# Kernel tuning notes

Measured on AMD Instinct MI355X. Metric: run time of the kernel, lower is better.

## Reference

```python
import jax, jax.numpy as jnp
import numpy as np

N_NODES = 100000
N_EDGES = 1600000
D = 128
NEG_SLOPE = 0.01  # torch F.leaky_relu default


def setup_inputs() -> dict:
    key = jax.random.key(0)
    k1, k2, k3, k4, k5, k6 = jax.random.split(key, 6)
    input = jax.random.normal(k1, (N_NODES, D), dtype=jnp.float32)
    edge_row = jax.random.randint(k2, (N_EDGES,), 0, N_NODES, dtype=jnp.int32)
    edge_col = jax.random.randint(k3, (N_EDGES,), 0, N_NODES, dtype=jnp.int32)
    edge_val = jax.random.uniform(k4, (N_EDGES,), dtype=jnp.float32)
    # learned params: W1: Linear(D, D, bias=False), W2: Linear(2D, D, bias=False)
    # torch stores weight as [out, in]; apply as x @ W.T
    bound1 = 1.0 / np.sqrt(D)
    bound2 = 1.0 / np.sqrt(2 * D)
    W1 = jax.random.uniform(k5, (D, D), dtype=jnp.float32, minval=-bound1, maxval=bound1)
    W2 = jax.random.uniform(k6, (D, 2 * D), dtype=jnp.float32, minval=-bound2, maxval=bound2)
    return {"input": input, "edge_row": edge_row, "edge_col": edge_col,
            "edge_val": edge_val, "W1": W1, "W2": W2}


def reference(input, edge_row, edge_col, edge_val, W1, W2):
    # proj_input = W1(input)
    proj = input @ W1.T                                   # [N, D]
    # neighboor = spmm(adj, proj): out[i] = sum_e val[e] * proj[col[e]] for row[e]==i
    msg = edge_val[:, None] * proj[edge_col]              # [E, D]
    neigh = jax.ops.segment_sum(msg, edge_row, num_segments=input.shape[0])  # [N, D]
    h = jnp.concatenate([input + neigh, input * neigh], axis=-1)  # [N, 2D]
    return jax.nn.leaky_relu(h @ W2.T, NEG_SLOPE)         # [N, D]
```

## Files before the change

### kernel.cpp

```cpp
#include <hip/hip_runtime.h>

#define DIM 128
#define BROWS 128
#define BCAP 3072
#define BK_EDGES 2048

typedef __attribute__((ext_vector_type(8))) short short8;
typedef __attribute__((ext_vector_type(4))) float f32x4;

__device__ __forceinline__ unsigned short f2bf(float f) {
    unsigned u = __float_as_uint(f);
    u += 0x7fffu + ((u >> 16) & 1u);
    return (unsigned short)(u >> 16);
}
__device__ __forceinline__ float bf2f(unsigned short b) {
    return __uint_as_float(((unsigned)b) << 16);
}

__global__ void k_pre(const float4* __restrict__ in, const float* __restrict__ W1,
                      const float* __restrict__ W2, unsigned short* __restrict__ inputb,
                      unsigned short* __restrict__ w1b, unsigned short* __restrict__ w2b,
                      int* __restrict__ gcur, int n4, int nCvt, int nbuk) {
    int b = blockIdx.x;
    if (b < nCvt) {
        int i = b * 256 + threadIdx.x;
        if (i < n4) {
            float4 v = in[i];
            *(ushort4*)(inputb + (long)i * 4) =
                make_ushort4(f2bf(v.x), f2bf(v.y), f2bf(v.z), f2bf(v.w));
        }
    } else if (b < nCvt + 192) {
        int idx = (b - nCvt) * 256 + threadIdx.x;
        if (idx < 16384)      w1b[idx] = f2bf(W1[idx]);
        else                  w2b[idx - 16384] = f2bf(W2[idx - 16384]);
    } else {
        int i = (b - nCvt - 192) * 256 + threadIdx.x;
        if (i < nbuk) gcur[i] = 0;
    }
}

__global__ __launch_bounds__(256) void k_bucket(const int* __restrict__ er,
                                                const int* __restrict__ ec,
                                                const float* __restrict__ ev,
                                                int* __restrict__ gcur,
                                                int2* __restrict__ edata, int E, int nbuk) {
    __shared__ int lhist[800];
    __shared__ int lpos[800];
    for (int b = threadIdx.x; b < nbuk; b += 256) lhist[b] = 0;
    __syncthreads();
    int e0 = blockIdx.x * BK_EDGES;
    for (int j = 0; j < BK_EDGES; j += 256) {
        int e = e0 + j + threadIdx.x;
        if (e < E) atomicAdd(&lhist[er[e] >> 7], 1);
    }
    __syncthreads();
    for (int b = threadIdx.x; b < nbuk; b += 256) {
        int c = lhist[b];
        int g = (c > 0) ? atomicAdd(&gcur[b], c) : 0;
        lpos[b] = b * BCAP + g;
    }
    __syncthreads();
    for (int j = 0; j < BK_EDGES; j += 256) {
        int e = e0 + j + threadIdx.x;
        if (e < E) {
            int r = er[e], b = r >> 7;
            int p = atomicAdd(&lpos[b], 1);
            if (p < (b + 1) * BCAP)
                edata[p] = make_int2(((r & 127) << 17) | ec[e], __float_as_int(ev[e]));
        }
    }
}

__global__ __launch_bounds__(256) void k_csr(int2* __restrict__ edata,
                                             const int* __restrict__ gcur,
                                             int* __restrict__ rs, int* __restrict__ re) {
    __shared__ int2 sed[BCAP];
    __shared__ int hist[BROWS];
    __shared__ int scan[BROWS];
    __shared__ int lcur[BROWS];
    int b = blockIdx.x, tid = threadIdx.x;
    int cnt = gcur[b]; if (cnt > BCAP) cnt = BCAP;
    int2* ed = edata + (long)b * BCAP;
    if (tid < BROWS) hist[tid] = 0;
    for (int i = tid; i < cnt; i += 256) sed[i] = ed[i];
    __syncthreads();
    for (int i = tid; i < cnt; i += 256) atomicAdd(&hist[sed[i].x >> 17], 1);
    __syncthreads();
    if (tid < BROWS) scan[tid] = hist[tid];
    __syncthreads();
    for (int off = 1; off < BROWS; off <<= 1) {
        int v = (tid < BROWS && tid >= off) ? scan[tid - off] : 0;
        __syncthreads();
        if (tid < BROWS) scan[tid] += v;
        __syncthreads();
    }
    if (tid < BROWS) {
        int excl = scan[tid] - hist[tid];
        lcur[tid] = excl;
        int row = b * BROWS + tid;
        rs[row] = b * BCAP + excl;
        re[row] = b * BCAP + excl + hist[tid];
    }
    __syncthreads();
    for (int i = tid; i < cnt; i += 256) {
        int2 v = sed[i];
        int p = atomicAdd(&lcur[v.x >> 17], 1);
        ed[p] = make_int2(v.x & 0x1FFFF, v.y);
    }
}

__global__ __launch_bounds__(256) void k_gather(const unsigned short* __restrict__ xb,
                                                const int2* __restrict__ edata,
                                                const int* __restrict__ rs,
                                                const int* __restrict__ re,
                                                unsigned short* __restrict__ aggb, int N) {
    int tid = threadIdx.x, lane = tid & 63, wave = tid >> 6;
    int grp = lane >> 4, s = lane & 15;
    int row = blockIdx.x * 16 + wave * 4 + grp;
    int beg = 0, end = 0;
    if (row < N) { beg = rs[row]; end = re[row]; }
    int deg = end - beg;
    int m = deg;
    m = max(m, __shfl_xor(m, 16));
    m = max(m, __shfl_xor(m, 32));
    float pa[8];
#pragma unroll
    for (int k = 0; k < 8; ++k) pa[k] = 0.f;
    const int4* x4 = (const int4*)xb;
    int bsrc = lane & 48;

#define ACC8(U, V)                                                         \
    {                                                                      \
        const unsigned* wp_ = (const unsigned*)&(U);                       \
        pa[0] += (V) * __uint_as_float(wp_[0] << 16);                      \
        pa[1] += (V) * __uint_as_float(wp_[0] & 0xffff0000u);              \
        pa[2] += (V) * __uint_as_float(wp_[1] << 16);                      \
        pa[3] += (V) * __uint_as_float(wp_[1] & 0xffff0000u);              \
        pa[4] += (V) * __uint_as_float(wp_[2] << 16);                      \
        pa[5] += (V) * __uint_as_float(wp_[2] & 0xffff0000u);              \
        pa[6] += (V) * __uint_as_float(wp_[3] << 16);                      \
        pa[7] += (V) * __uint_as_float(wp_[3] & 0xffff0000u);              \
    }

    for (int c0 = 0; c0 < m; c0 += 16) {
        int idx = beg + c0 + s;
        int2 ed = (idx < end) ? edata[idx] : make_int2(0, 0);
        int nc = m - c0; if (nc > 16) nc = 16;
        nc = (nc + 3) & ~3;
        for (int j = 0; j < nc; j += 4) {
            int cx0 = __shfl(ed.x, bsrc + j);
            int cx1 = __shfl(ed.x, bsrc + j + 1);
            int cx2 = __shfl(ed.x, bsrc + j + 2);
            int cx3 = __shfl(ed.x, bsrc + j + 3);
            float v0 = __int_as_float(__shfl(ed.y, bsrc + j));
            float v1 = __int_as_float(__shfl(ed.y, bsrc + j + 1));
            float v2 = __int_as_float(__shfl(ed.y, bsrc + j + 2));
            float v3 = __int_as_float(__shfl(ed.y, bsrc + j + 3));
            int4 u0 = x4[(long)cx0 * 16 + s];
            int4 u1 = x4[(long)cx1 * 16 + s];
            int4 u2 = x4[(long)cx2 * 16 + s];
            int4 u3 = x4[(long)cx3 * 16 + s];
            ACC8(u0, v0);
            ACC8(u1, v1);
            ACC8(u2, v2);
            ACC8(u3, v3);
        }
    }
#undef ACC8

    if (row < N) {
        short8 o;
#pragma unroll
        for (int k = 0; k < 8; ++k) o[k] = (short)f2bf(pa[k]);
        *(short8*)(aggb + (long)row * DIM + s * 8) = o;
    }
}

__global__ __launch_bounds__(256, 4) void k_fused(const unsigned short* __restrict__ aggb,
                                                  const unsigned short* __restrict__ inputb,
                                                  const unsigned short* __restrict__ w1b,
                                                  const unsigned short* __restrict__ w2b,
                                                  float* __restrict__ out, int N) {
    __shared__ __align__(16) unsigned short sh[2 * 64 * 136];
    int w = threadIdx.x >> 6, lane = threadIdx.x & 63;
    int quad = lane >> 4, lq = lane & 15;
    int blk0 = blockIdx.x * 64;
    unsigned short* sh0 = sh;
    unsigned short* sh1 = sh + 64 * 136;

    short8 b1[2][4];
#pragma unroll
    for (int ntl = 0; ntl < 2; ++ntl)
#pragma unroll
        for (int kb = 0; kb < 4; ++kb)
            b1[ntl][kb] = *(const short8*)(w1b + ((w * 2 + ntl) * 16 + lq) * DIM +
                                           kb * 32 + quad * 8);

#pragma unroll
    for (int mt = 0; mt < 4; ++mt) {
        short8 afr[4];
        {
            int row = blk0 + mt * 16 + lq; if (row >= N) row = N - 1;
#pragma unroll
            for (int kb = 0; kb < 4; ++kb)
                afr[kb] = *(const short8*)(aggb + (long)row * DIM + kb * 32 + quad * 8);
        }
#pragma unroll
        for (int ntl = 0; ntl < 2; ++ntl) {
            f32x4 c = {0.f, 0.f, 0.f, 0.f};
#pragma unroll
            for (int kb = 0; kb < 4; ++kb)
                c = __builtin_amdgcn_mfma_f32_16x16x32_bf16(afr[kb], b1[ntl][kb], c, 0, 0, 0);
            int nt = w * 2 + ntl;
#pragma unroll
            for (int rg = 0; rg < 4; ++rg) {
                int r = blk0 + mt * 16 + quad * 4 + rg;
                int rr = (r < N) ? r : (N - 1);
                float x = bf2f(inputb[(long)rr * DIM + nt * 16 + lq]);
                float nb = c[rg];
                int off = (mt * 16 + quad * 4 + rg) * 136 + nt * 16 + lq;
                sh0[off] = f2bf(x + nb);
                sh1[off] = f2bf(x * nb);
            }
        }
    }

    short8 b2[2][8];
#pragma unroll
    for (int ntl = 0; ntl < 2; ++ntl)
#pragma unroll
        for (int kb = 0; kb < 8; ++kb)
            b2[ntl][kb] = *(const short8*)(w2b + ((w * 2 + ntl) * 16 + lq) * 256 +
                                           kb * 32 + quad * 8);
    __syncthreads();

#pragma unroll
    for (int mt = 0; mt < 4; ++mt) {
        int arow = (mt * 16 + lq) * 136;
        short8 a0[4], a1[4];
#pragma unroll
        for (int kb = 0; kb < 4; ++kb) {
            a0[kb] = *(const short8*)(sh0 + arow + kb * 32 + quad * 8);
            a1[kb] = *(const short8*)(sh1 + arow + kb * 32 + quad * 8);
        }
#pragma unroll
        for (int ntl = 0; ntl < 2; ++ntl) {
            f32x4 c = {0.f, 0.f, 0.f, 0.f};
#pragma unroll
            for (int kb = 0; kb < 4; ++kb)
                c = __builtin_amdgcn_mfma_f32_16x16x32_bf16(a0[kb], b2[ntl][kb], c, 0, 0, 0);
#pragma unroll
            for (int kb = 0; kb < 4; ++kb)
                c = __builtin_amdgcn_mfma_f32_16x16x32_bf16(a1[kb], b2[ntl][kb + 4], c, 0, 0, 0);
            int nt = w * 2 + ntl;
#pragma unroll
            for (int rg = 0; rg < 4; ++rg) {
                int r = blk0 + mt * 16 + quad * 4 + rg;
                if (r < N) {
                    float v = c[rg];
                    v = (v > 0.f) ? v : 0.01f * v;
                    out[(long)r * DIM + nt * 16 + lq] = v;
                }
            }
        }
    }
}

extern "C" void kernel_launch(void* const* d_in, const int* in_sizes, int n_in,
                              void* d_out, int out_size, void* d_ws, size_t ws_size,
                              hipStream_t stream) {
    const float* input = (const float*)d_in[0];
    const int*   er    = (const int*)d_in[1];
    const int*   ec    = (const int*)d_in[2];
    const float* ev    = (const float*)d_in[3];
    const float* W1    = (const float*)d_in[4];
    const float* W2    = (const float*)d_in[5];
    int N = in_sizes[0] / DIM;
    int E = in_sizes[1];
    float* out = (float*)d_out;
    int nbuk = (N + BROWS - 1) / BROWS;

    int* ws = (int*)d_ws;
    int* gcur = ws;
    int2* edata = (int2*)(ws + 1024);
    int* rs = (int*)(edata + (long)nbuk * BCAP);
    int* re = rs + (long)nbuk * BROWS;
    unsigned short* w1b = (unsigned short*)(re + (long)nbuk * BROWS);
    unsigned short* w2b = w1b + 16384;
    unsigned short* inputb = w2b + 32768;
    unsigned short* aggb = inputb + (long)N * DIM;

    int n4 = N * (DIM / 4);
    int nCvt = (n4 + 255) / 256;
    int nZero = (nbuk + 255) / 256;
    k_pre<<<nCvt + 192 + nZero, 256, 0, stream>>>(
        (const float4*)input, W1, W2, inputb, w1b, w2b, gcur, n4, nCvt, nbuk);

    k_bucket<<<(E + BK_EDGES - 1) / BK_EDGES, 256, 0, stream>>>(
        er, ec, ev, gcur, edata, E, nbuk);

    k_csr<<<nbuk, 256, 0, stream>>>(edata, gcur, rs, re);

    k_gather<<<(N + 15) / 16, 256, 0, stream>>>(inputb, edata, rs, re, aggb, N);

    k_fused<<<(N + 63) / 64, 256, 0, stream>>>(aggb, inputb, w1b, w2b, out, N);
}
```

Baseline: 275.9 us.

## Use coarse 1024-row buckets and compact CSR output into dense edge array

Edges are now bucketed by groups of 1024 rows (98 buckets) into a temporary staging area that aliases the aggregation buffer. The CSR kernel then runs with 1024 threads per bucket and computes each bucket's global base with a serial prefix over the bucket counts. It scatters edges into a compact, densely packed edge array instead of padded per-bucket slots. This cuts global atomic contention and shrinks the bucket-histogram work, and it gives the gather kernel contiguous edges. The costs are far fewer CSR blocks (98, so low occupancy), per-thread global re-reads instead of shared-memory staging, and reliance on a fixed bucket capacity that may overflow on skewed inputs.

```diff
diff --git a/kernel.cpp b/kernel.cpp
--- a/kernel.cpp
+++ b/kernel.cpp
@@ -1,8 +1,8 @@
 #include <hip/hip_runtime.h>
 
 #define DIM 128
-#define BROWS 128
-#define BCAP 3072
+#define CB_ROWS 1024
+#define CCAP 18432
 #define BK_EDGES 2048
 
 typedef __attribute__((ext_vector_type(8))) short short8;
@@ -43,69 +43,76 @@
                                                 const int* __restrict__ ec,
                                                 const float* __restrict__ ev,
                                                 int* __restrict__ gcur,
-                                                int2* __restrict__ edata, int E, int nbuk) {
-    __shared__ int lhist[800];
-    __shared__ int lpos[800];
-    for (int b = threadIdx.x; b < nbuk; b += 256) lhist[b] = 0;
+                                                int2* __restrict__ edata0, int E, int nbuk) {
+    __shared__ int lhist[128];
+    __shared__ int lpos[128];
+    if (threadIdx.x < 128) lhist[threadIdx.x] = 0;
     __syncthreads();
     int e0 = blockIdx.x * BK_EDGES;
     for (int j = 0; j < BK_EDGES; j += 256) {
         int e = e0 + j + threadIdx.x;
-        if (e < E) atomicAdd(&lhist[er[e] >> 7], 1);
-    }
-    __syncthreads();
-    for (int b = threadIdx.x; b < nbuk; b += 256) {
-        int c = lhist[b];
-        int g = (c > 0) ? atomicAdd(&gcur[b], c) : 0;
-        lpos[b] = b * BCAP + g;
+        if (e < E) atomicAdd(&lhist[er[e] >> 10], 1);
+    }
+    __syncthreads();
+    if (threadIdx.x < nbuk) {
+        int c = lhist[threadIdx.x];
+        int g = (c > 0) ? atomicAdd(&gcur[threadIdx.x], c) : 0;
+        lpos[threadIdx.x] = threadIdx.x * CCAP + g;
     }
     __syncthreads();
     for (int j = 0; j < BK_EDGES; j += 256) {
         int e = e0 + j + threadIdx.x;
         if (e < E) {
-            int r = er[e], b = r >> 7;
+            int r = er[e], b = r >> 10;
             int p = atomicAdd(&lpos[b], 1);
-            if (p < (b + 1) * BCAP)
-                edata[p] = make_int2(((r & 127) << 17) | ec[e], __float_as_int(ev[e]));
-        }
-    }
-}
-
-__global__ __launch_bounds__(256) void k_csr(int2* __restrict__ edata,
-                                             const int* __restrict__ gcur,
-                                             int* __restrict__ rs, int* __restrict__ re) {
-    __shared__ int2 sed[BCAP];
-    __shared__ int hist[BROWS];
-    __shared__ int scan[BROWS];
-    __shared__ int lcur[BROWS];
+            if (p < (b + 1) * CCAP)
+                edata0[p] = make_int2(((r & 1023) << 17) | ec[e], __float_as_int(ev[e]));
+        }
+    }
+}
+
+__global__ __launch_bounds__(1024) void k_csr(const int2* __restrict__ edata0,
+                                              const int* __restrict__ gcur,
+                                              int2* __restrict__ edata,
+                                              int* __restrict__ rs, int* __restrict__ re,
+                                              int N, int nbuk) {
+    __shared__ int hist[CB_ROWS];
+    __shared__ int scan[CB_ROWS];
+    __shared__ int lcur[CB_ROWS];
+    __shared__ int cbuf[128];
+    __shared__ int cbase;
     int b = blockIdx.x, tid = threadIdx.x;
-    int cnt = gcur[b]; if (cnt > BCAP) cnt = BCAP;
-    int2* ed = edata + (long)b * BCAP;
-    if (tid < BROWS) hist[tid] = 0;
-    for (int i = tid; i < cnt; i += 256) sed[i] = ed[i];
-    __syncthreads();
-    for (int i = tid; i < cnt; i += 256) atomicAdd(&hist[sed[i].x >> 17], 1);
-    __syncthreads();
-    if (tid < BROWS) scan[tid] = hist[tid];
-    __syncthreads();
-    for (int off = 1; off < BROWS; off <<= 1) {
-        int v = (tid < BROWS && tid >= off) ? scan[tid - off] : 0;
+    if (tid < nbuk) { int c = gcur[tid]; cbuf[tid] = (c > CCAP) ? CCAP : c; }
+    hist[tid] = 0;
+    __syncthreads();
+    if (tid == 0) {
+        int s = 0;
+        for (int i = 0; i < b; ++i) s += cbuf[i];
+        cbase = s;
+    }
+    __syncthreads();
+    int base = cbase;
+    int cnt = cbuf[b];
+    const int2* e0 = edata0 + (long)b * CCAP;
+    for (int i = tid; i < cnt; i += 1024) atomicAdd(&hist[e0[i].x >> 17], 1);
+    __syncthreads();
+    scan[tid] = hist[tid];
+    __syncthreads();
+    for (int off = 1; off < CB_ROWS; off <<= 1) {
+        int v = (tid >= off) ? scan[tid - off] : 0;
         __syncthreads();
-        if (tid < BROWS) scan[tid] += v;
+        scan[tid] += v;
         __syncthreads();
     }
-    if (tid < BROWS) {
-        int excl = scan[tid] - hist[tid];
-        lcur[tid] = excl;
-        int row = b * BROWS + tid;
-        rs[row] = b * BCAP + excl;
-        re[row] = b * BCAP + excl + hist[tid];
-    }
-    __syncthreads();
-    for (int i = tid; i < cnt; i += 256) {
-        int2 v = sed[i];
+    int excl = scan[tid] - hist[tid];
+    lcur[tid] = base + excl;
+    int row = b * CB_ROWS + tid;
+    if (row < N) { rs[row] = base + excl; re[row] = base + excl + hist[tid]; }
+    __syncthreads();
+    for (int i = tid; i < cnt; i += 1024) {
+        int2 v = e0[i];
         int p = atomicAdd(&lcur[v.x >> 17], 1);
-        ed[p] = make_int2(v.x & 0x1FFFF, v.y);
+        edata[p] = make_int2(v.x & 0x1FFFF, v.y);
     }
 }
 
@@ -278,17 +285,18 @@
     int N = in_sizes[0] / DIM;
     int E = in_sizes[1];
     float* out = (float*)d_out;
-    int nbuk = (N + BROWS - 1) / BROWS;
+    int nbuk = (N + CB_ROWS - 1) / CB_ROWS;
 
     int* ws = (int*)d_ws;
     int* gcur = ws;
     int2* edata = (int2*)(ws + 1024);
-    int* rs = (int*)(edata + (long)nbuk * BCAP);
-    int* re = rs + (long)nbuk * BROWS;
-    unsigned short* w1b = (unsigned short*)(re + (long)nbuk * BROWS);
+    int* rs = (int*)(edata + (long)E);
+    int* re = rs + N;
+    unsigned short* w1b = (unsigned short*)(re + N);
     unsigned short* w2b = w1b + 16384;
     unsigned short* inputb = w2b + 32768;
     unsigned short* aggb = inputb + (long)N * DIM;
+    int2* edata0 = (int2*)aggb;
 
     int n4 = N * (DIM / 4);
     int nCvt = (n4 + 255) / 256;
@@ -297,9 +305,9 @@
         (const float4*)input, W1, W2, inputb, w1b, w2b, gcur, n4, nCvt, nbuk);
 
     k_bucket<<<(E + BK_EDGES - 1) / BK_EDGES, 256, 0, stream>>>(
-        er, ec, ev, gcur, edata, E, nbuk);
-
-    k_csr<<<nbuk, 256, 0, stream>>>(edata, gcur, rs, re);
+        er, ec, ev, gcur, edata0, E, nbuk);
+
+    k_csr<<<nbuk, 1024, 0, stream>>>(edata0, gcur, edata, rs, re, N, nbuk);
 
     k_gather<<<(N + 15) / 16, 256, 0, stream>>>(inputb, edata, rs, re, aggb, N);
 
```

Measured after the change: 276.9 us. Within noise of the previous version (+0.4%).

## Fuse CSR build into gather and stage bucket writes through shared memory

Applied to the files above, without the earlier changes.

The bucketing kernel now uses 1024-thread blocks over 6144 edges. It locally sorts edges by bucket in LDS via a prefix scan, then writes each bucket's run contiguously to global memory for coalesced stores. The separate CSR kernel is removed. Its per-row sort now runs inside the gather kernel, which keeps the sorted edge list in LDS and processes all 128 rows of a bucket per block. This drops one launch and the global round-trip of rs/re and reordered edata, at the cost of only nbuk (~782) gather blocks with serialized per-row loops, which may reduce parallelism and load balance.

```diff
diff --git a/kernel.cpp b/kernel.cpp
--- a/kernel.cpp
+++ b/kernel.cpp
@@ -3,7 +3,8 @@
 #define DIM 128
 #define BROWS 128
 #define BCAP 3072
-#define BK_EDGES 2048
+#define NBUK_PAD 800
+#define BK_EDGES 6144
 
 typedef __attribute__((ext_vector_type(8))) short short8;
 typedef __attribute__((ext_vector_type(4))) float f32x4;
@@ -39,95 +40,92 @@
     }
 }
 
-__global__ __launch_bounds__(256) void k_bucket(const int* __restrict__ er,
-                                                const int* __restrict__ ec,
-                                                const float* __restrict__ ev,
-                                                int* __restrict__ gcur,
-                                                int2* __restrict__ edata, int E, int nbuk) {
-    __shared__ int lhist[800];
-    __shared__ int lpos[800];
-    for (int b = threadIdx.x; b < nbuk; b += 256) lhist[b] = 0;
+__global__ __launch_bounds__(1024) void k_bucket(const int* __restrict__ er,
+                                                 const int* __restrict__ ec,
+                                                 const float* __restrict__ ev,
+                                                 int* __restrict__ gcur,
+                                                 int2* __restrict__ edata0, int E, int nbuk) {
+    __shared__ int2 sed[BK_EDGES];
+    __shared__ int lhist[NBUK_PAD];
+    __shared__ int lscan[NBUK_PAD];
+    __shared__ int lpos[NBUK_PAD];
+    __shared__ int gbase[NBUK_PAD];
+    int tid = threadIdx.x;
+    if (tid < NBUK_PAD) lhist[tid] = 0;
     __syncthreads();
     int e0 = blockIdx.x * BK_EDGES;
-    for (int j = 0; j < BK_EDGES; j += 256) {
-        int e = e0 + j + threadIdx.x;
-        if (e < E) atomicAdd(&lhist[er[e] >> 7], 1);
-    }
-    __syncthreads();
-    for (int b = threadIdx.x; b < nbuk; b += 256) {
-        int c = lhist[b];
-        int g = (c > 0) ? atomicAdd(&gcur[b], c) : 0;
-        lpos[b] = b * BCAP + g;
-    }
-    __syncthreads();
-    for (int j = 0; j < BK_EDGES; j += 256) {
-        int e = e0 + j + threadIdx.x;
-        if (e < E) {
-            int r = er[e], b = r >> 7;
-            int p = atomicAdd(&lpos[b], 1);
-            if (p < (b + 1) * BCAP)
-                edata[p] = make_int2(((r & 127) << 17) | ec[e], __float_as_int(ev[e]));
-        }
-    }
-}
-
-__global__ __launch_bounds__(256) void k_csr(int2* __restrict__ edata,
-                                             const int* __restrict__ gcur,
-                                             int* __restrict__ rs, int* __restrict__ re) {
+    int bcnt = E - e0; if (bcnt > BK_EDGES) bcnt = BK_EDGES;
+    for (int i = tid; i < bcnt; i += 1024)
+        atomicAdd(&lhist[er[e0 + i] >> 7], 1);
+    __syncthreads();
+    if (tid < NBUK_PAD) lscan[tid] = lhist[tid];
+    __syncthreads();
+    for (int off = 1; off < NBUK_PAD; off <<= 1) {
+        int v = (tid < NBUK_PAD && tid >= off) ? lscan[tid - off] : 0;
+        __syncthreads();
+        if (tid < NBUK_PAD) lscan[tid] += v;
+        __syncthreads();
+    }
+    if (tid < NBUK_PAD) {
+        int c = lhist[tid];
+        lpos[tid] = lscan[tid] - c;
+        gbase[tid] = (c > 0 && tid < nbuk) ? atomicAdd(&gcur[tid], c) : 0;
+    }
+    __syncthreads();
+    for (int i = tid; i < bcnt; i += 1024) {
+        int e = e0 + i;
+        int r = er[e], bk = r >> 7;
+        int p = atomicAdd(&lpos[bk], 1);
+        sed[p] = make_int2(((r & 127) << 17) | ec[e], __float_as_int(ev[e]));
+    }
+    __syncthreads();
+    int wv = tid >> 6, lane = tid & 63;
+    for (int bk = wv; bk < nbuk; bk += 16) {
+        int c = lhist[bk];
+        if (c == 0) continue;
+        int excl = lscan[bk] - c;
+        int gb = gbase[bk];
+        long base = (long)bk * BCAP;
+        for (int j = lane; j < c; j += 64)
+            if (gb + j < BCAP)
+                edata0[base + gb + j] = sed[excl + j];
+    }
+}
+
+__global__ __launch_bounds__(256) void k_gather(const unsigned short* __restrict__ xb,
+                                                const int2* __restrict__ edata0,
+                                                const int* __restrict__ gcur,
+                                                unsigned short* __restrict__ aggb, int N) {
     __shared__ int2 sed[BCAP];
     __shared__ int hist[BROWS];
-    __shared__ int scan[BROWS];
+    __shared__ int hscan[BROWS];
     __shared__ int lcur[BROWS];
-    int b = blockIdx.x, tid = threadIdx.x;
+    int tid = threadIdx.x, b = blockIdx.x;
     int cnt = gcur[b]; if (cnt > BCAP) cnt = BCAP;
-    int2* ed = edata + (long)b * BCAP;
+    const int2* e0 = edata0 + (long)b * BCAP;
     if (tid < BROWS) hist[tid] = 0;
-    for (int i = tid; i < cnt; i += 256) sed[i] = ed[i];
-    __syncthreads();
-    for (int i = tid; i < cnt; i += 256) atomicAdd(&hist[sed[i].x >> 17], 1);
-    __syncthreads();
-    if (tid < BROWS) scan[tid] = hist[tid];
+    __syncthreads();
+    for (int i = tid; i < cnt; i += 256) atomicAdd(&hist[e0[i].x >> 17], 1);
+    __syncthreads();
+    if (tid < BROWS) hscan[tid] = hist[tid];
     __syncthreads();
     for (int off = 1; off < BROWS; off <<= 1) {
-        int v = (tid < BROWS && tid >= off) ? scan[tid - off] : 0;
+        int v = (tid < BROWS && tid >= off) ? hscan[tid - off] : 0;
         __syncthreads();
-        if (tid < BROWS) scan[tid] += v;
+        if (tid < BROWS) hscan[tid] += v;
         __syncthreads();
     }
-    if (tid < BROWS) {
-        int excl = scan[tid] - hist[tid];
-        lcur[tid] = excl;
-        int row = b * BROWS + tid;
-        rs[row] = b * BCAP + excl;
-        re[row] = b * BCAP + excl + hist[tid];
-    }
+    if (tid < BROWS) lcur[tid] = hscan[tid] - hist[tid];
     __syncthreads();
     for (int i = tid; i < cnt; i += 256) {
-        int2 v = sed[i];
+        int2 v = e0[i];
         int p = atomicAdd(&lcur[v.x >> 17], 1);
-        ed[p] = make_int2(v.x & 0x1FFFF, v.y);
-    }
-}
-
-__global__ __launch_bounds__(256) void k_gather(const unsigned short* __restrict__ xb,
-                                                const int2* __restrict__ edata,
-                                                const int* __restrict__ rs,
-                                                const int* __restrict__ re,
-                                                unsigned short* __restrict__ aggb, int N) {
-    int tid = threadIdx.x, lane = tid & 63, wave = tid >> 6;
-    int grp = lane >> 4, s = lane & 15;
-    int row = blockIdx.x * 16 + wave * 4 + grp;
-    int beg = 0, end = 0;
-    if (row < N) { beg = rs[row]; end = re[row]; }
-    int deg = end - beg;
-    int m = deg;
-    m = max(m, __shfl_xor(m, 16));
-    m = max(m, __shfl_xor(m, 32));
-    float pa[8];
-#pragma unroll
-    for (int k = 0; k < 8; ++k) pa[k] = 0.f;
+        sed[p] = make_int2(v.x & 0x1FFFF, v.y);
+    }
+    __syncthreads();
+
+    int slot = tid >> 4, s = tid & 15;
     const int4* x4 = (const int4*)xb;
-    int bsrc = lane & 48;
 
 #define ACC8(U, V)                                                         \
     {                                                                      \
@@ -142,38 +140,41 @@
         pa[7] += (V) * __uint_as_float(wp_[3] & 0xffff0000u);              \
     }
 
-    for (int c0 = 0; c0 < m; c0 += 16) {
-        int idx = beg + c0 + s;
-        int2 ed = (idx < end) ? edata[idx] : make_int2(0, 0);
-        int nc = m - c0; if (nc > 16) nc = 16;
-        nc = (nc + 3) & ~3;
-        for (int j = 0; j < nc; j += 4) {
-            int cx0 = __shfl(ed.x, bsrc + j);
-            int cx1 = __shfl(ed.x, bsrc + j + 1);
-            int cx2 = __shfl(ed.x, bsrc + j + 2);
-            int cx3 = __shfl(ed.x, bsrc + j + 3);
-            float v0 = __int_as_float(__shfl(ed.y, bsrc + j));
-            float v1 = __int_as_float(__shfl(ed.y, bsrc + j + 1));
-            float v2 = __int_as_float(__shfl(ed.y, bsrc + j + 2));
-            float v3 = __int_as_float(__shfl(ed.y, bsrc + j + 3));
-            int4 u0 = x4[(long)cx0 * 16 + s];
-            int4 u1 = x4[(long)cx1 * 16 + s];
-            int4 u2 = x4[(long)cx2 * 16 + s];
-            int4 u3 = x4[(long)cx3 * 16 + s];
+    for (int k = 0; k < 8; ++k) {
+        int rl = k * 16 + slot;
+        int row = b * BROWS + rl;
+        int beg = hscan[rl] - hist[rl], end = hscan[rl];
+        float pa[8];
+#pragma unroll
+        for (int t = 0; t < 8; ++t) pa[t] = 0.f;
+        int j = beg;
+        for (; j + 4 <= end; j += 4) {
+            int2 q0 = sed[j], q1 = sed[j + 1], q2 = sed[j + 2], q3 = sed[j + 3];
+            int4 u0 = x4[(long)q0.x * 16 + s];
+            int4 u1 = x4[(long)q1.x * 16 + s];
+            int4 u2 = x4[(long)q2.x * 16 + s];
+            int4 u3 = x4[(long)q3.x * 16 + s];
+            float v0 = __int_as_float(q0.y), v1 = __int_as_float(q1.y);
+            float v2 = __int_as_float(q2.y), v3 = __int_as_float(q3.y);
             ACC8(u0, v0);
             ACC8(u1, v1);
             ACC8(u2, v2);
             ACC8(u3, v3);
         }
+        for (; j < end; ++j) {
+            int2 q = sed[j];
+            int4 u = x4[(long)q.x * 16 + s];
+            float v = __int_as_float(q.y);
+            ACC8(u, v);
+        }
+        if (row < N) {
+            short8 o;
+#pragma unroll
+            for (int t = 0; t < 8; ++t) o[t] = (short)f2bf(pa[t]);
+            *(short8*)(aggb + (long)row * DIM + s * 8) = o;
+        }
     }
 #undef ACC8
-
-    if (row < N) {
-        short8 o;
-#pragma unroll
-        for (int k = 0; k < 8; ++k) o[k] = (short)f2bf(pa[k]);
-        *(short8*)(aggb + (long)row * DIM + s * 8) = o;
-    }
 }
 
 __global__ __launch_bounds__(256, 4) void k_fused(const unsigned short* __restrict__ aggb,
@@ -282,10 +283,8 @@
 
     int* ws = (int*)d_ws;
     int* gcur = ws;
-    int2* edata = (int2*)(ws + 1024);
-    int* rs = (int*)(edata + (long)nbuk * BCAP);
-    int* re = rs + (long)nbuk * BROWS;
-    unsigned short* w1b = (unsigned short*)(re + (long)nbuk * BROWS);
+    int2* edata0 = (int2*)(ws + 1024);
+    unsigned short* w1b = (unsigned short*)(edata0 + (long)nbuk * BCAP);
     unsigned short* w2b = w1b + 16384;
     unsigned short* inputb = w2b + 32768;
     unsigned short* aggb = inputb + (long)N * DIM;
@@ -296,12 +295,10 @@
     k_pre<<<nCvt + 192 + nZero, 256, 0, stream>>>(
         (const float4*)input, W1, W2, inputb, w1b, w2b, gcur, n4, nCvt, nbuk);
 
-    k_bucket<<<(E + BK_EDGES - 1) / BK_EDGES, 256, 0, stream>>>(
-        er, ec, ev, gcur, edata, E, nbuk);
-
-    k_csr<<<nbuk, 256, 0, stream>>>(edata, gcur, rs, re);
-
-    k_gather<<<(N + 15) / 16, 256, 0, stream>>>(inputb, edata, rs, re, aggb, N);
+    k_bucket<<<(E + BK_EDGES - 1) / BK_EDGES, 1024, 0, stream>>>(
+        er, ec, ev, gcur, edata0, E, nbuk);
+
+    k_gather<<<nbuk, 256, 0, stream>>>(inputb, edata0, gcur, aggb, N);
 
     k_fused<<<(N + 63) / 64, 256, 0, stream>>>(aggb, inputb, w1b, w2b, out, N);
 }
```

Result: faster. 249.8 us (-9.5%).
